# Performance work log

Measured on AMD Instinct MI355X. Metric: run time of the kernel, lower is better.

## Reference

```python
import jax, jax.numpy as jnp
import numpy as np
from jax import lax

GRID_X, GRID_Y = 8, 8
CELL = 48  # cell_pixel_size
BATCH = 64


def setup_inputs() -> dict:
    key = jax.random.key(0)
    ks = jax.random.split(key, 9)
    s = lambda *sh: 1.0 / np.sqrt(np.prod(sh[1:])) if len(sh) > 1 else 0.0
    inp = {
        "x": jax.random.normal(ks[0], (BATCH, 3, GRID_X * CELL, GRID_Y * CELL), jnp.float32),
        "conv1_w": jax.random.normal(ks[1], (16, 3, 8, 8), jnp.float32) * 0.05,
        "conv1_b": jax.random.normal(ks[2], (16,), jnp.float32) * 0.05,
        "conv2_w": jax.random.normal(ks[3], (32, 16, 4, 4), jnp.float32) * 0.05,
        "conv2_b": jax.random.normal(ks[4], (32,), jnp.float32) * 0.05,
        "fc1_w": jax.random.normal(ks[5], (256, 288), jnp.float32) * 0.05,
        "fc1_b": jax.random.normal(ks[6], (256,), jnp.float32) * 0.05,
        "fc2_w": jax.random.normal(ks[7], (4, 256), jnp.float32) * 0.05,
        "fc2_b": jax.random.normal(ks[8], (4,), jnp.float32) * 0.05,
    }
    return inp


def _conv(x, w, b, stride, pad):
    y = lax.conv_general_dilated(
        x, w, window_strides=(stride, stride),
        padding=[(pad, pad), (pad, pad)],
        dimension_numbers=("NCHW", "OIHW", "NCHW"))
    return y + b[None, :, None, None]


def reference(x, conv1_w, conv1_b, conv2_w, conv2_b, fc1_w, fc1_b, fc2_w, fc2_b):
    B = x.shape[0]
    num_cells = GRID_X * GRID_Y
    # Grid extraction: one strided reshape instead of per-cell crop loop.
    # [B,3,gx*CELL,gy*CELL] -> [B,gx,gy,3,CELL,CELL] -> [B*cells,3,CELL,CELL]
    cells = x.reshape(B, 3, GRID_X, CELL, GRID_Y, CELL)
    cells = cells.transpose(0, 2, 4, 1, 3, 5).reshape(B * num_cells, 3, CELL, CELL)
    h = jax.nn.relu(_conv(cells, conv1_w, conv1_b, stride=4, pad=2))  # [N,16,12,12]
    h = jax.nn.relu(_conv(h, conv2_w, conv2_b, stride=4, pad=1))      # [N,32,3,3]
    h = h.reshape(B * num_cells, -1)                                   # [N,288]
    h = jax.nn.relu(h @ fc1_w.T + fc1_b)
    logits = h @ fc2_w.T + fc2_b
    probs = jax.nn.softmax(logits, axis=1)
    feats = probs.reshape(B, num_cells, 4)
    return (feats[:, :, 0], feats[:, :, 1], feats[:, :, 2])
```

## Files before the change

### kernel.cpp

```cpp
#include <hip/hip_runtime.h>

typedef float f32x4 __attribute__((ext_vector_type(4)));
typedef short s16x8 __attribute__((ext_vector_type(8)));

#define NT 512

#define CB_ROW 52
#define CB_PLANE 2704
#define CB_CELL 8112
#define H1_CI 208
#define H1_CELL 3328
#define W2_STR 264
#define H2_STR 296
#define H3_STR 260

__device__ __forceinline__ ushort f2bf(float f) {
  unsigned u = __float_as_uint(f);
  unsigned r = (u + 0x7fffu + ((u >> 16) & 1u)) >> 16;
  return (ushort)r;
}

__device__ __forceinline__ int cellbase4(int n) {
  int b = n >> 6, gg = n & 63;
  return b * 110592 + (gg >> 3) * 4608 + (gg & 7) * 12;
}

__global__ void prep_kernel(const float* __restrict__ fw1, ushort* __restrict__ fw1b) {
  int i = blockIdx.x * 256 + threadIdx.x;
  fw1b[i] = f2bf(fw1[i]);
}

__global__ __launch_bounds__(NT, 4)
void fused_kernel(const float* __restrict__ x,
                  const float* __restrict__ w1, const float* __restrict__ b1,
                  const float* __restrict__ w2, const float* __restrict__ b2,
                  const ushort* __restrict__ fw1b, const float* __restrict__ fb1,
                  const float* __restrict__ fw2, const float* __restrict__ fb2,
                  float* __restrict__ out)
{
  __shared__ __align__(16) ushort cb[2 * CB_CELL];
  __shared__ __align__(16) ushort h1[2 * H1_CELL];
  __shared__ __align__(16) ushort w2t[32 * W2_STR];
  __shared__ __align__(16) ushort h2[16 * H2_STR];
  __shared__ __align__(16) float  h3[8 * H3_STR];
  __shared__ float ls[8][4];

  const int t = threadIdx.x;
  const int w = t >> 6;
  const int lane = t & 63;
  const int r16 = lane & 15;
  const int g = lane >> 4;

  int cls[7], goff[7], eoff[7];
#pragma unroll
  for (int i = 0; i < 7; ++i) {
    int q = i * NT + t;
    bool valid = q < 3456;
    int qq = valid ? q : 0;
    int cl = qq >= 1728 ? 1 : 0;
    int rem = qq - cl * 1728;
    int c = rem / 576; int r2 = rem - c * 576;
    int y = r2 / 12;   int quad = r2 - y * 12;
    cls[i] = valid ? cl : -1;
    goff[i] = c * 36864 + y * 96 + quad;
    eoff[i] = cl * CB_CELL + c * CB_PLANE + (y + 2) * CB_ROW + 2 + quad * 4;
  }

  const int cell00 = blockIdx.x * 8;
  const float4* x4 = (const float4*)x;

  float4 v[7];
  {
    int b0 = cellbase4(cell00), b1_ = cellbase4(cell00 + 1);
#pragma unroll
    for (int i = 0; i < 7; ++i)
      if (cls[i] >= 0) v[i] = x4[(cls[i] ? b1_ : b0) + goff[i]];
  }

  for (int i = t; i < CB_CELL; i += NT) ((uint*)cb)[i] = 0u;
  for (int i = t; i < H1_CELL; i += NT) ((uint*)h1)[i] = 0u;
  for (int i = t; i < 2368; i += NT) ((uint*)h2)[i] = 0u;
  for (int i = t; i < 8192; i += NT) {
    int oc = i >> 8, k = i & 255;
    w2t[oc * W2_STR + k] = f2bf(w2[i]);
  }

  s16x8 b1f[6];
#pragma unroll
  for (int s = 0; s < 6; ++s) {
    const float* p = w1 + r16 * 192 + s * 32 + g * 8;
    float4 lo = *(const float4*)p;
    float4 hi = *(const float4*)(p + 4);
    s16x8 vv;
    vv[0] = (short)f2bf(lo.x); vv[1] = (short)f2bf(lo.y);
    vv[2] = (short)f2bf(lo.z); vv[3] = (short)f2bf(lo.w);
    vv[4] = (short)f2bf(hi.x); vv[5] = (short)f2bf(hi.y);
    vv[6] = (short)f2bf(hi.z); vv[7] = (short)f2bf(hi.w);
    b1f[s] = vv;
  }
  const float b1v = b1[r16];
  const float b2v = b2[(w & 1) * 16 + r16];

  const int mtbase = w & 3;
  const int clA = w >> 2;
  int rowA[3];
#pragma unroll
  for (int ii = 0; ii < 3; ++ii) {
    int mt = mtbase + ii * 4;
    int m = (mt < 9 ? mt : 0) * 16 + r16;
    int oy = m / 12, ox = m - 12 * oy;
    rowA[ii] = oy * 208 + 4 * ox;
  }
  const int pcl = r16 < 9 ? r16 : 8;
  const int p2y = pcl / 3, p2x = pcl - 3 * p2y;
  const int lco = (g >> 1) * H1_CI + (4 * p2y + 2 * (g & 1)) * 16 + 4 * p2x;
  const int cellC = (w >> 1) & 1, ntC = w & 1;

  __syncthreads();

  for (int rnd = 0; rnd < 4; ++rnd) {
#pragma unroll
    for (int i = 0; i < 7; ++i)
      if (cls[i] >= 0) {
        float4 q = v[i]; int e = eoff[i];
        *(uint*)&cb[e]     = (uint)f2bf(q.x) | ((uint)f2bf(q.y) << 16);
        *(uint*)&cb[e + 2] = (uint)f2bf(q.z) | ((uint)f2bf(q.w) << 16);
      }
    __syncthreads();

    f32x4 acc[3];
#pragma unroll
    for (int ii = 0; ii < 3; ++ii) acc[ii] = (f32x4){0.f, 0.f, 0.f, 0.f};
    const ushort* cbc = cb + clA * CB_CELL;
#pragma unroll
    for (int s = 0; s < 6; ++s) {
      int sbase = (s >> 1) * CB_PLANE + ((s & 1) * 4 + g) * CB_ROW;
#pragma unroll
      for (int ii = 0; ii < 3; ++ii) {
        if (mtbase + ii * 4 < 9) {
          int e = sbase + rowA[ii];
          s16x8 a;
          ((uint2*)&a)[0] = *(const uint2*)&cbc[e];
          ((uint2*)&a)[1] = *(const uint2*)&cbc[e + 4];
          acc[ii] = __builtin_amdgcn_mfma_f32_16x16x32_bf16(a, b1f[s], acc[ii], 0, 0, 0);
        }
      }
    }
    {
      ushort* h1c = h1 + clA * H1_CELL;
#pragma unroll
      for (int ii = 0; ii < 3; ++ii) {
        int mt = mtbase + ii * 4;
        if (mt < 9) {
#pragma unroll
          for (int rr = 0; rr < 4; ++rr) {
            int m = mt * 16 + g * 4 + rr;
            int oy = m / 12, ox = m - 12 * oy;
            float val = fmaxf(acc[ii][rr] + b1v, 0.f);
            h1c[r16 * H1_CI + (oy + 1) * 16 + (ox + 1)] = f2bf(val);
          }
        }
      }
    }

    if (rnd < 3) {
      int n0 = cell00 + (rnd + 1) * 2;
      int b0 = cellbase4(n0), b1_ = cellbase4(n0 + 1);
#pragma unroll
      for (int i = 0; i < 7; ++i)
        if (cls[i] >= 0) v[i] = x4[(cls[i] ? b1_ : b0) + goff[i]];
    }
    __syncthreads();

    if (w < 4) {
      const ushort* h1cc = h1 + cellC * H1_CELL;
      f32x4 a2 = (f32x4){0.f, 0.f, 0.f, 0.f};
#pragma unroll
      for (int s2 = 0; s2 < 8; ++s2) {
        int off = s2 * 416 + lco;
        s16x8 a;
        ((uint2*)&a)[0] = *(const uint2*)&h1cc[off];
        ((uint2*)&a)[1] = *(const uint2*)&h1cc[off + 16];
        uint4 qb = *(const uint4*)&w2t[(ntC * 16 + r16) * W2_STR + s2 * 32 + g * 8];
        a2 = __builtin_amdgcn_mfma_f32_16x16x32_bf16(a, *(s16x8*)&qb, a2, 0, 0, 0);
      }
#pragma unroll
      for (int rr = 0; rr < 4; ++rr) {
        int m2 = g * 4 + rr;
        if (m2 < 9) {
          float val = fmaxf(a2[rr] + b2v, 0.f);
          h2[(rnd * 2 + cellC) * H2_STR + (ntC * 16 + r16) * 9 + m2] = f2bf(val);
        }
      }
    }
  }
  __syncthreads();

  {
    s16x8 af[9];
#pragma unroll
    for (int s = 0; s < 9; ++s) {
      uint4 qa = *(const uint4*)&h2[r16 * H2_STR + s * 32 + g * 8];
      af[s] = *(s16x8*)&qa;
    }
    f32x4 fa0 = (f32x4){0.f, 0.f, 0.f, 0.f};
    f32x4 fa1 = (f32x4){0.f, 0.f, 0.f, 0.f};
#pragma unroll
    for (int s = 0; s < 9; ++s) {
      uint4 q0 = *(const uint4*)(fw1b + ((2 * w) * 16 + r16) * 288 + s * 32 + g * 8);
      fa0 = __builtin_amdgcn_mfma_f32_16x16x32_bf16(af[s], *(s16x8*)&q0, fa0, 0, 0, 0);
      uint4 q1 = *(const uint4*)(fw1b + ((2 * w + 1) * 16 + r16) * 288 + s * 32 + g * 8);
      fa1 = __builtin_amdgcn_mfma_f32_16x16x32_bf16(af[s], *(s16x8*)&q1, fa1, 0, 0, 0);
    }
#pragma unroll
    for (int i = 0; i < 2; ++i) {
      f32x4 fa = i ? fa1 : fa0;
      int n = (2 * w + i) * 16 + r16;
      float fb = fb1[n];
#pragma unroll
      for (int rr = 0; rr < 4; ++rr) {
        int cell = g * 4 + rr;
        if (cell < 8) h3[cell * H3_STR + n] = fmaxf(fa[rr] + fb, 0.f);
      }
    }
  }
  __syncthreads();

  {
    int u = t >> 4, sub = t & 15;
    int cell = u >> 2, j = u & 3;
    const float4* hp = (const float4*)&h3[cell * H3_STR];
    const float4* wp = (const float4*)(fw2 + j * 256);
    float p = 0.f;
#pragma unroll
    for (int i = 0; i < 4; ++i) {
      int k4 = sub + i * 16;
      float4 a = hp[k4], b = wp[k4];
      p = fmaf(a.x, b.x, p); p = fmaf(a.y, b.y, p);
      p = fmaf(a.z, b.z, p); p = fmaf(a.w, b.w, p);
    }
    p += __shfl_xor(p, 1);
    p += __shfl_xor(p, 2);
    p += __shfl_xor(p, 4);
    p += __shfl_xor(p, 8);
    if (sub == 0) ls[cell][j] = p + fb2[j];
  }
  __syncthreads();

  if (t < 8) {
    float l0 = ls[t][0], l1 = ls[t][1], l2 = ls[t][2], l3 = ls[t][3];
    float m = fmaxf(fmaxf(l0, l1), fmaxf(l2, l3));
    float e0 = __expf(l0 - m), e1 = __expf(l1 - m),
          e2 = __expf(l2 - m), e3 = __expf(l3 - m);
    float inv = 1.f / (e0 + e1 + e2 + e3);
    int n = cell00 + t;
    out[n] = e0 * inv;
    out[4096 + n] = e1 * inv;
    out[8192 + n] = e2 * inv;
  }
}

extern "C" void kernel_launch(void* const* d_in, const int* in_sizes, int n_in,
                              void* d_out, int out_size, void* d_ws, size_t ws_size,
                              hipStream_t stream) {
  const float* x   = (const float*)d_in[0];
  const float* w1  = (const float*)d_in[1];
  const float* b1  = (const float*)d_in[2];
  const float* w2  = (const float*)d_in[3];
  const float* b2  = (const float*)d_in[4];
  const float* fw1 = (const float*)d_in[5];
  const float* fb1 = (const float*)d_in[6];
  const float* fw2 = (const float*)d_in[7];
  const float* fb2 = (const float*)d_in[8];
  float* out = (float*)d_out;
  ushort* fw1b = (ushort*)d_ws;

  hipLaunchKernelGGL(prep_kernel, dim3(288), dim3(256), 0, stream, fw1, fw1b);
  hipLaunchKernelGGL(fused_kernel, dim3(512), dim3(NT), 0, stream,
                     x, w1, b1, w2, b2, fw1b, fb1, fw2, fb2, out);
}
```

Measured before the change: 50.86 us.

## Process four cells per block with one cell per round to shrink LDS and double grid

Each block now handles four cells, one per round, instead of eight cells two at a time, and the grid grows to 1024 blocks. LDS buffers are cut to a single cell, and h3 and the logits scratch reuse the input-cell buffer, so more blocks can be resident; launch bounds are raised to 6. Conv1 work is redistributed so each wave does one M tile plus a rotating ninth tile. The register prefetch of the next cell is dropped, which exposes global load latency, and each block repeats the w2 conversion and setup per four cells instead of eight.

```diff
diff --git a/kernel.cpp b/kernel.cpp
--- a/kernel.cpp
+++ b/kernel.cpp
@@ -4,15 +4,10 @@
 typedef short s16x8 __attribute__((ext_vector_type(8)));
 
 #define NT 512
-
 #define CB_ROW 52
 #define CB_PLANE 2704
-#define CB_CELL 8112
-#define H1_CI 208
-#define H1_CELL 3328
+#define H1_CI 192
 #define W2_STR 264
-#define H2_STR 296
-#define H3_STR 260
 
 __device__ __forceinline__ ushort f2bf(float f) {
   unsigned u = __float_as_uint(f);
@@ -30,7 +25,7 @@
   fw1b[i] = f2bf(fw1[i]);
 }
 
-__global__ __launch_bounds__(NT, 4)
+__global__ __launch_bounds__(NT, 6)
 void fused_kernel(const float* __restrict__ x,
                   const float* __restrict__ w1, const float* __restrict__ b1,
                   const float* __restrict__ w2, const float* __restrict__ b2,
@@ -38,12 +33,12 @@
                   const float* __restrict__ fw2, const float* __restrict__ fb2,
                   float* __restrict__ out)
 {
-  __shared__ __align__(16) ushort cb[2 * CB_CELL];
-  __shared__ __align__(16) ushort h1[2 * H1_CELL];
-  __shared__ __align__(16) ushort w2t[32 * W2_STR];
-  __shared__ __align__(16) ushort h2[16 * H2_STR];
-  __shared__ __align__(16) float  h3[8 * H3_STR];
-  __shared__ float ls[8][4];
+  __shared__ __align__(16) ushort cb[8112];
+  __shared__ __align__(16) ushort h1[3072];
+  __shared__ __align__(16) ushort h2[4608];
+  __shared__ __align__(16) ushort w2t[8448];
+  float* h3 = (float*)cb;
+  float* lsp = (float*)cb + 1040;
 
   const int t = threadIdx.x;
   const int w = t >> 6;
@@ -51,35 +46,20 @@
   const int r16 = lane & 15;
   const int g = lane >> 4;
 
-  int cls[7], goff[7], eoff[7];
-#pragma unroll
-  for (int i = 0; i < 7; ++i) {
+  int goff[4], eoff[4];
+#pragma unroll
+  for (int i = 0; i < 4; ++i) {
     int q = i * NT + t;
-    bool valid = q < 3456;
-    int qq = valid ? q : 0;
-    int cl = qq >= 1728 ? 1 : 0;
-    int rem = qq - cl * 1728;
-    int c = rem / 576; int r2 = rem - c * 576;
-    int y = r2 / 12;   int quad = r2 - y * 12;
-    cls[i] = valid ? cl : -1;
+    int qq = q < 1728 ? q : 0;
+    int c = qq / 576; int r2 = qq - c * 576;
+    int y = r2 / 12;  int quad = r2 - y * 12;
     goff[i] = c * 36864 + y * 96 + quad;
-    eoff[i] = cl * CB_CELL + c * CB_PLANE + (y + 2) * CB_ROW + 2 + quad * 4;
-  }
-
-  const int cell00 = blockIdx.x * 8;
-  const float4* x4 = (const float4*)x;
-
-  float4 v[7];
-  {
-    int b0 = cellbase4(cell00), b1_ = cellbase4(cell00 + 1);
-#pragma unroll
-    for (int i = 0; i < 7; ++i)
-      if (cls[i] >= 0) v[i] = x4[(cls[i] ? b1_ : b0) + goff[i]];
-  }
-
-  for (int i = t; i < CB_CELL; i += NT) ((uint*)cb)[i] = 0u;
-  for (int i = t; i < H1_CELL; i += NT) ((uint*)h1)[i] = 0u;
-  for (int i = t; i < 2368; i += NT) ((uint*)h2)[i] = 0u;
+    eoff[i] = c * CB_PLANE + (y + 2) * CB_ROW + 2 + quad * 4;
+  }
+
+  for (int i = t; i < 4056; i += NT) ((uint*)cb)[i] = 0u;
+  for (int i = t; i < 1536; i += NT) ((uint*)h1)[i] = 0u;
+  for (int i = t; i < 2304; i += NT) ((uint*)h2)[i] = 0u;
   for (int i = t; i < 8192; i += NT) {
     int oc = i >> 8, k = i & 255;
     w2t[oc * W2_STR + k] = f2bf(w2[i]);
@@ -101,95 +81,95 @@
   const float b1v = b1[r16];
   const float b2v = b2[(w & 1) * 16 + r16];
 
-  const int mtbase = w & 3;
-  const int clA = w >> 2;
-  int rowA[3];
-#pragma unroll
-  for (int ii = 0; ii < 3; ++ii) {
-    int mt = mtbase + ii * 4;
-    int m = (mt < 9 ? mt : 0) * 16 + r16;
-    int oy = m / 12, ox = m - 12 * oy;
-    rowA[ii] = oy * 208 + 4 * ox;
-  }
+  const int m_w = w * 16 + r16;
+  const int rowA_w = (m_w / 12) * (4 * CB_ROW) + 4 * (m_w % 12);
+  const int m_8 = 128 + r16;
+  const int rowA_8 = (m_8 / 12) * (4 * CB_ROW) + 4 * (m_8 % 12);
+
   const int pcl = r16 < 9 ? r16 : 8;
   const int p2y = pcl / 3, p2x = pcl - 3 * p2y;
   const int lco = (g >> 1) * H1_CI + (4 * p2y + 2 * (g & 1)) * 16 + 4 * p2x;
-  const int cellC = (w >> 1) & 1, ntC = w & 1;
-
-  __syncthreads();
+  const int ntC = w & 1;
+  const int w2base = (ntC * 16 + r16) * W2_STR;
+
+  __syncthreads();
+
+  const int cell0 = blockIdx.x * 4;
+  const float4* x4 = (const float4*)x;
 
   for (int rnd = 0; rnd < 4; ++rnd) {
-#pragma unroll
-    for (int i = 0; i < 7; ++i)
-      if (cls[i] >= 0) {
-        float4 q = v[i]; int e = eoff[i];
-        *(uint*)&cb[e]     = (uint)f2bf(q.x) | ((uint)f2bf(q.y) << 16);
-        *(uint*)&cb[e + 2] = (uint)f2bf(q.z) | ((uint)f2bf(q.w) << 16);
-      }
+    {
+      int base = cellbase4(cell0 + rnd);
+      float4 vv[4];
+#pragma unroll
+      for (int i = 0; i < 4; ++i)
+        if (i < 3 || t < 192) vv[i] = x4[base + goff[i]];
+#pragma unroll
+      for (int i = 0; i < 4; ++i)
+        if (i < 3 || t < 192) {
+          float4 q = vv[i]; int e = eoff[i];
+          *(uint*)&cb[e]     = (uint)f2bf(q.x) | ((uint)f2bf(q.y) << 16);
+          *(uint*)&cb[e + 2] = (uint)f2bf(q.z) | ((uint)f2bf(q.w) << 16);
+        }
+    }
     __syncthreads();
 
-    f32x4 acc[3];
-#pragma unroll
-    for (int ii = 0; ii < 3; ++ii) acc[ii] = (f32x4){0.f, 0.f, 0.f, 0.f};
-    const ushort* cbc = cb + clA * CB_CELL;
+    const bool has8 = (w == ((2 * rnd + 4) & 7));
+    f32x4 a0 = (f32x4){0.f, 0.f, 0.f, 0.f};
+    f32x4 a8 = (f32x4){0.f, 0.f, 0.f, 0.f};
 #pragma unroll
     for (int s = 0; s < 6; ++s) {
       int sbase = (s >> 1) * CB_PLANE + ((s & 1) * 4 + g) * CB_ROW;
-#pragma unroll
-      for (int ii = 0; ii < 3; ++ii) {
-        if (mtbase + ii * 4 < 9) {
-          int e = sbase + rowA[ii];
-          s16x8 a;
-          ((uint2*)&a)[0] = *(const uint2*)&cbc[e];
-          ((uint2*)&a)[1] = *(const uint2*)&cbc[e + 4];
-          acc[ii] = __builtin_amdgcn_mfma_f32_16x16x32_bf16(a, b1f[s], acc[ii], 0, 0, 0);
-        }
-      }
-    }
-    {
-      ushort* h1c = h1 + clA * H1_CELL;
-#pragma unroll
-      for (int ii = 0; ii < 3; ++ii) {
-        int mt = mtbase + ii * 4;
-        if (mt < 9) {
-#pragma unroll
-          for (int rr = 0; rr < 4; ++rr) {
-            int m = mt * 16 + g * 4 + rr;
-            int oy = m / 12, ox = m - 12 * oy;
-            float val = fmaxf(acc[ii][rr] + b1v, 0.f);
-            h1c[r16 * H1_CI + (oy + 1) * 16 + (ox + 1)] = f2bf(val);
-          }
-        }
-      }
-    }
-
-    if (rnd < 3) {
-      int n0 = cell00 + (rnd + 1) * 2;
-      int b0 = cellbase4(n0), b1_ = cellbase4(n0 + 1);
-#pragma unroll
-      for (int i = 0; i < 7; ++i)
-        if (cls[i] >= 0) v[i] = x4[(cls[i] ? b1_ : b0) + goff[i]];
+      s16x8 a;
+      ((uint2*)&a)[0] = *(const uint2*)&cb[sbase + rowA_w];
+      ((uint2*)&a)[1] = *(const uint2*)&cb[sbase + rowA_w + 4];
+      a0 = __builtin_amdgcn_mfma_f32_16x16x32_bf16(a, b1f[s], a0, 0, 0, 0);
+    }
+    if (has8) {
+#pragma unroll
+      for (int s = 0; s < 6; ++s) {
+        int sbase = (s >> 1) * CB_PLANE + ((s & 1) * 4 + g) * CB_ROW;
+        s16x8 a;
+        ((uint2*)&a)[0] = *(const uint2*)&cb[sbase + rowA_8];
+        ((uint2*)&a)[1] = *(const uint2*)&cb[sbase + rowA_8 + 4];
+        a8 = __builtin_amdgcn_mfma_f32_16x16x32_bf16(a, b1f[s], a8, 0, 0, 0);
+      }
+    }
+#pragma unroll
+    for (int rr = 0; rr < 4; ++rr) {
+      int m = w * 16 + g * 4 + rr;
+      int oy = m / 12, ox = m - 12 * oy;
+      if (oy < 11 && ox < 11)
+        h1[r16 * H1_CI + (oy + 1) * 16 + (ox + 1)] = f2bf(fmaxf(a0[rr] + b1v, 0.f));
+    }
+    if (has8) {
+#pragma unroll
+      for (int rr = 0; rr < 4; ++rr) {
+        int m = 128 + g * 4 + rr;
+        int oy = m / 12, ox = m - 12 * oy;
+        if (oy < 11 && ox < 11)
+          h1[r16 * H1_CI + (oy + 1) * 16 + (ox + 1)] = f2bf(fmaxf(a8[rr] + b1v, 0.f));
+      }
     }
     __syncthreads();
 
-    if (w < 4) {
-      const ushort* h1cc = h1 + cellC * H1_CELL;
-      f32x4 a2 = (f32x4){0.f, 0.f, 0.f, 0.f};
+    if ((w >> 1) == rnd) {
+      f32x4 c2 = (f32x4){0.f, 0.f, 0.f, 0.f};
 #pragma unroll
       for (int s2 = 0; s2 < 8; ++s2) {
-        int off = s2 * 416 + lco;
+        int off = s2 * 384 + lco;
         s16x8 a;
-        ((uint2*)&a)[0] = *(const uint2*)&h1cc[off];
-        ((uint2*)&a)[1] = *(const uint2*)&h1cc[off + 16];
-        uint4 qb = *(const uint4*)&w2t[(ntC * 16 + r16) * W2_STR + s2 * 32 + g * 8];
-        a2 = __builtin_amdgcn_mfma_f32_16x16x32_bf16(a, *(s16x8*)&qb, a2, 0, 0, 0);
+        ((uint2*)&a)[0] = *(const uint2*)&h1[off];
+        ((uint2*)&a)[1] = *(const uint2*)&h1[off + 16];
+        uint4 qb = *(const uint4*)&w2t[w2base + s2 * 32 + g * 8];
+        c2 = __builtin_amdgcn_mfma_f32_16x16x32_bf16(a, *(s16x8*)&qb, c2, 0, 0, 0);
       }
 #pragma unroll
       for (int rr = 0; rr < 4; ++rr) {
         int m2 = g * 4 + rr;
         if (m2 < 9) {
-          float val = fmaxf(a2[rr] + b2v, 0.f);
-          h2[(rnd * 2 + cellC) * H2_STR + (ntC * 16 + r16) * 9 + m2] = f2bf(val);
+          float val = fmaxf(c2[rr] + b2v, 0.f);
+          h2[rnd * 288 + (ntC * 16 + r16) * 9 + m2] = f2bf(val);
         }
       }
     }
@@ -200,7 +180,7 @@
     s16x8 af[9];
 #pragma unroll
     for (int s = 0; s < 9; ++s) {
-      uint4 qa = *(const uint4*)&h2[r16 * H2_STR + s * 32 + g * 8];
+      uint4 qa = *(const uint4*)&h2[r16 * 288 + s * 32 + g * 8];
       af[s] = *(s16x8*)&qa;
     }
     f32x4 fa0 = (f32x4){0.f, 0.f, 0.f, 0.f};
@@ -220,21 +200,21 @@
 #pragma unroll
       for (int rr = 0; rr < 4; ++rr) {
         int cell = g * 4 + rr;
-        if (cell < 8) h3[cell * H3_STR + n] = fmaxf(fa[rr] + fb, 0.f);
+        if (cell < 4) h3[cell * 260 + n] = fmaxf(fa[rr] + fb, 0.f);
       }
     }
   }
   __syncthreads();
 
   {
-    int u = t >> 4, sub = t & 15;
+    int u = t >> 5, sub = t & 31;
     int cell = u >> 2, j = u & 3;
-    const float4* hp = (const float4*)&h3[cell * H3_STR];
+    const float4* hp = (const float4*)&h3[cell * 260];
     const float4* wp = (const float4*)(fw2 + j * 256);
     float p = 0.f;
 #pragma unroll
-    for (int i = 0; i < 4; ++i) {
-      int k4 = sub + i * 16;
+    for (int i = 0; i < 2; ++i) {
+      int k4 = sub + 32 * i;
       float4 a = hp[k4], b = wp[k4];
       p = fmaf(a.x, b.x, p); p = fmaf(a.y, b.y, p);
       p = fmaf(a.z, b.z, p); p = fmaf(a.w, b.w, p);
@@ -243,17 +223,19 @@
     p += __shfl_xor(p, 2);
     p += __shfl_xor(p, 4);
     p += __shfl_xor(p, 8);
-    if (sub == 0) ls[cell][j] = p + fb2[j];
-  }
-  __syncthreads();
-
-  if (t < 8) {
-    float l0 = ls[t][0], l1 = ls[t][1], l2 = ls[t][2], l3 = ls[t][3];
+    p += __shfl_xor(p, 16);
+    if (sub == 0) lsp[cell * 4 + j] = p + fb2[j];
+  }
+  __syncthreads();
+
+  if (t < 4) {
+    float l0 = lsp[t * 4 + 0], l1 = lsp[t * 4 + 1],
+          l2 = lsp[t * 4 + 2], l3 = lsp[t * 4 + 3];
     float m = fmaxf(fmaxf(l0, l1), fmaxf(l2, l3));
     float e0 = __expf(l0 - m), e1 = __expf(l1 - m),
           e2 = __expf(l2 - m), e3 = __expf(l3 - m);
     float inv = 1.f / (e0 + e1 + e2 + e3);
-    int n = cell00 + t;
+    int n = cell0 + t;
     out[n] = e0 * inv;
     out[4096 + n] = e1 * inv;
     out[8192 + n] = e2 * inv;
@@ -276,6 +258,6 @@
   ushort* fw1b = (ushort*)d_ws;
 
   hipLaunchKernelGGL(prep_kernel, dim3(288), dim3(256), 0, stream, fw1, fw1b);
-  hipLaunchKernelGGL(fused_kernel, dim3(512), dim3(NT), 0, stream,
+  hipLaunchKernelGGL(fused_kernel, dim3(1024), dim3(NT), 0, stream,
                      x, w1, b1, w2, b2, fw1b, fb1, fw2, fb2, out);
 }
```

Result: slower. 59.76 us (+17.5%).
